# Optimization experiments

Measured on AMD Instinct MI355X. Metric: run time of the kernel, lower is better.

## Reference

```python
import jax, jax.numpy as jnp
import numpy as np

DMODEL = 1024
NHEAD = 16
DHEAD = DMODEL // NHEAD

def _layernorm(x, g, b, eps=1e-5):
    mu = jnp.mean(x, axis=-1, keepdims=True)
    var = jnp.var(x, axis=-1, keepdims=True)
    return (x - mu) * jax.lax.rsqrt(var + eps) * g + b

def setup_inputs() -> dict:
    key = jax.random.key(0)
    ks = jax.random.split(key, 12)
    b, lq, lv, d = 2, 2048, 2048, DMODEL
    s = 1.0 / np.sqrt(d)
    return {
        "q": jax.random.normal(ks[0], (b, lq, d), jnp.float32),
        "k": jax.random.normal(ks[1], (b, lv, d), jnp.float32),
        "v": jax.random.normal(ks[2], (b, lv, d), jnp.float32),
        "qln_g": jnp.ones((d,), jnp.float32),
        "qln_b": jnp.zeros((d,), jnp.float32),
        "kvln_g": jnp.ones((d,), jnp.float32),
        "kvln_b": jnp.zeros((d,), jnp.float32),
        "Wq": jax.random.normal(ks[3], (d, d), jnp.float32) * s,
        "Wk": jax.random.normal(ks[4], (d, d), jnp.float32) * s,
        "Wv": jax.random.normal(ks[5], (d, d), jnp.float32) * s,
        "Wg": jax.random.normal(ks[6], (d, d), jnp.float32) * s,
        "bg": jnp.zeros((d,), jnp.float32),
        "Wo": jax.random.normal(ks[7], (d, d), jnp.float32) * s,
    }

def reference(q, k, v, qln_g, qln_b, kvln_g, kvln_b, Wq, Wk, Wv, Wg, bg, Wo):
    b, lq, d = q.shape
    lv = v.shape[1]
    qn = _layernorm(q, qln_g, qln_b)           # [b, lq, d]
    q_ = qn @ Wq.T
    kk = _layernorm(k, kvln_g, kvln_b) @ Wk.T
    vv = _layernorm(v, kvln_g, kvln_b) @ Wv.T
    qh = q_.reshape(b, lq, NHEAD, DHEAD)       # bqhd
    kh = kk.reshape(b, lv, NHEAD, DHEAD)
    vh = vv.reshape(b, lv, NHEAD, DHEAD)
    scores = jnp.einsum('bqhd,bkhd->bhqk', qh, kh) / np.sqrt(DHEAD)
    attn = jax.nn.softmax(scores, axis=-1)
    y = jnp.einsum('bhqk,bkhd->bqhd', attn, vh).reshape(b, lq, d)
    g = jax.nn.sigmoid(qn @ Wg.T + bg)
    return (y * g) @ Wo.T
```

## Files before the change

kernel.cpp:

```cpp
#include <hip/hip_runtime.h>
#include <hip/hip_bf16.h>

#define DMODEL 1024
#define NHEAD  16
#define DHEAD  64
#define BATCH  2
#define LQ     2048
#define LV     2048
#define ROWS   (BATCH*LQ)
#define WELEMS (DMODEL*DMODEL)
#define BH     (BATCH*NHEAD)

typedef short bf16x8 __attribute__((ext_vector_type(8)));
typedef float f32x4  __attribute__((ext_vector_type(4)));

__device__ __forceinline__ float bf2f(unsigned short s) {
    union { unsigned u; float f; } v; v.u = ((unsigned)s) << 16;
    return v.f;
}
__device__ __forceinline__ unsigned pk_bf(float a, float b) {
    union { __hip_bfloat162 h; unsigned u; } c;
    c.h = __float22bfloat162_rn(make_float2(a, b));
    return c.u;
}

__device__ __forceinline__ void cp16_g2l(const void* g, void* l) {
    __builtin_amdgcn_global_load_lds(
        (const __attribute__((address_space(1))) void*)g,
        (__attribute__((address_space(3))) void*)l,
        16, 0, 0);
}

#define QSCALE (0.125f * 1.4426950408889634f)

__global__ __launch_bounds__(256) void prep_kernel(
    const float* q, const float* k, const float* v,
    const float* qg, const float* qb, const float* kvg, const float* kvb,
    const float* Wq, const float* Wk, const float* Wv, const float* Wg, const float* Wo,
    unsigned short* qn, unsigned short* kn, unsigned short* vn, unsigned short* wb)
{
    __shared__ float rs[4], rq[4];
    int z = blockIdx.y;
    if (z < 5) {
        if (blockIdx.x >= WELEMS / 1024) return;
        const float* srcs[5] = {Wq, Wk, Wv, Wg, Wo};
        const float* s = srcs[z];
        unsigned short* d = wb + (size_t)z * WELEMS;
        int i = (blockIdx.x * 256 + threadIdx.x) * 4;
        float4 x = *(const float4*)(s + i);
        uint2 o = make_uint2(pk_bf(x.x, x.y), pk_bf(x.z, x.w));
        *(uint2*)(d + i) = o;
        return;
    }
    int row = blockIdx.x;
    const float *x, *gp, *bp; unsigned short* o;
    if      (z == 5) { x = q; gp = qg;  bp = qb;  o = qn; }
    else if (z == 6) { x = k; gp = kvg; bp = kvb; o = kn; }
    else             { x = v; gp = kvg; bp = kvb; o = vn; }

    int col = threadIdx.x * 4;
    float4 xv = *(const float4*)(x + (size_t)row * DMODEL + col);
    float s  = xv.x + xv.y + xv.z + xv.w;
    float sq = xv.x*xv.x + xv.y*xv.y + xv.z*xv.z + xv.w*xv.w;
    #pragma unroll
    for (int off = 1; off < 64; off <<= 1) { s += __shfl_xor(s, off); sq += __shfl_xor(sq, off); }

    int wave = threadIdx.x >> 6, lane = threadIdx.x & 63;
    if (lane == 0) { rs[wave] = s; rq[wave] = sq; }
    __syncthreads();
    float ts = rs[0] + rs[1] + rs[2] + rs[3];
    float tq = rq[0] + rq[1] + rq[2] + rq[3];
    float mu  = ts * (1.0f / DMODEL);
    float var = tq * (1.0f / DMODEL) - mu * mu;
    float inv = rsqrtf(var + 1e-5f);

    float4 gv = *(const float4*)(gp + col);
    float4 bv = *(const float4*)(bp + col);
    float r0 = (xv.x - mu) * inv * gv.x + bv.x;
    float r1 = (xv.y - mu) * inv * gv.y + bv.y;
    float r2 = (xv.z - mu) * inv * gv.z + bv.z;
    float r3 = (xv.w - mu) * inv * gv.w + bv.w;
    *(uint2*)(o + (size_t)row * DMODEL + col) = make_uint2(pk_bf(r0, r1), pk_bf(r2, r3));
}

template<int MODE>
__device__ __forceinline__ void gemm256_core(
    const unsigned short* A, const unsigned short* Bw,
    unsigned short* Obf, const float* bias, float scale,
    unsigned short* Al, unsigned short* Bl, int bm, int bn)
{
    int tid  = threadIdx.x;
    int w = tid >> 6, l = tid & 63, quad = l >> 4, L = l & 15;
    int wm = w >> 2, wn = w & 3;

    int c16 = (l & 7) ^ (l >> 3);
    const unsigned short* gAs = A  + (size_t)(bm * 256 + w * 8 + (l >> 3)) * DMODEL + c16 * 8;
    const unsigned short* gBs = Bw + (size_t)(bn * 256 + w * 8 + (l >> 3)) * DMODEL + c16 * 8;
    int dstE = w * 512;

    #define STG_A2(t, ro) do { const unsigned short* s_ = gAs + (size_t)(ro) * DMODEL + (t) * 64; \
        unsigned short* d_ = Al + ((t) & 1) * 16384 + (ro) * 64 + dstE;                           \
        cp16_g2l(s_, d_); cp16_g2l(s_ + 64 * DMODEL, d_ + 4096); } while (0)
    #define STG_B2(t, ro) do { const unsigned short* s_ = gBs + (size_t)(ro) * DMODEL + (t) * 64; \
        unsigned short* d_ = Bl + ((t) & 1) * 16384 + (ro) * 64 + dstE;                           \
        cp16_g2l(s_, d_); cp16_g2l(s_ + 64 * DMODEL, d_ + 4096); } while (0)

    int sw = (L & 7) << 3;
    int o0 = (quad * 8) ^ sw;
    int o1 = (32 + quad * 8) ^ sw;

    f32x4 acc[8][4];
    #pragma unroll
    for (int i = 0; i < 8; ++i)
        #pragma unroll
        for (int j = 0; j < 4; ++j) acc[i][j] = (f32x4){0.f, 0.f, 0.f, 0.f};

    STG_A2(0, 0); STG_A2(0, 128); STG_B2(0, 0); STG_B2(0, 128);
    STG_A2(1, 0); STG_A2(1, 128);
    asm volatile("s_waitcnt vmcnt(4)" ::: "memory");
    __builtin_amdgcn_s_barrier();

    const int NT = DMODEL / 64;
    for (int t = 0; t < NT; ++t) {
        const unsigned short* Ab = Al + (t & 1) * 16384 + wm * 8192;
        const unsigned short* Bb = Bl + (t & 1) * 16384 + wn * 4096;
        bf16x8 b0[4], b1[4], a0[2], a1[2], r0v[6], r1v[6];

        #pragma unroll
        for (int j = 0; j < 4; ++j) {
            b0[j] = *(const bf16x8*)&Bb[(j * 16 + L) * 64 + o0];
            b1[j] = *(const bf16x8*)&Bb[(j * 16 + L) * 64 + o1];
        }
        #pragma unroll
        for (int i2 = 0; i2 < 2; ++i2) {
            a0[i2] = *(const bf16x8*)&Ab[(i2 * 16 + L) * 64 + o0];
            a1[i2] = *(const bf16x8*)&Ab[(i2 * 16 + L) * 64 + o1];
        }
        if (t + 1 < NT) STG_B2(t + 1, 0);
        __builtin_amdgcn_s_barrier();
        __builtin_amdgcn_s_setprio(1);
        #pragma unroll
        for (int i2 = 0; i2 < 2; ++i2)
            #pragma unroll
            for (int j = 0; j < 4; ++j) {
                if (MODE == 3) {
                    acc[i2][j] = __builtin_amdgcn_mfma_f32_16x16x32_bf16(a0[i2], b0[j], acc[i2][j], 0, 0, 0);
                    acc[i2][j] = __builtin_amdgcn_mfma_f32_16x16x32_bf16(a1[i2], b1[j], acc[i2][j], 0, 0, 0);
                } else {
                    acc[i2][j] = __builtin_amdgcn_mfma_f32_16x16x32_bf16(b0[j], a0[i2], acc[i2][j], 0, 0, 0);
                    acc[i2][j] = __builtin_amdgcn_mfma_f32_16x16x32_bf16(b1[j], a1[i2], acc[i2][j], 0, 0, 0);
                }
            }
        __builtin_amdgcn_s_setprio(0);
        __builtin_amdgcn_s_barrier();

        #pragma unroll
        for (int r = 0; r < 6; ++r) {
            r0v[r] = *(const bf16x8*)&Ab[((32 + r * 16) + L) * 64 + o0];
            r1v[r] = *(const bf16x8*)&Ab[((32 + r * 16) + L) * 64 + o1];
        }
        if (t + 1 < NT) STG_B2(t + 1, 128);
        __builtin_amdgcn_s_barrier();
        __builtin_amdgcn_s_setprio(1);
        #pragma unroll
        for (int i2 = 0; i2 < 2; ++i2)
            #pragma unroll
            for (int j = 0; j < 4; ++j) {
                if (MODE == 3) {
                    acc[2 + i2][j] = __builtin_amdgcn_mfma_f32_16x16x32_bf16(r0v[i2], b0[j], acc[2 + i2][j], 0, 0, 0);
                    acc[2 + i2][j] = __builtin_amdgcn_mfma_f32_16x16x32_bf16(r1v[i2], b1[j], acc[2 + i2][j], 0, 0, 0);
                } else {
                    acc[2 + i2][j] = __builtin_amdgcn_mfma_f32_16x16x32_bf16(b0[j], r0v[i2], acc[2 + i2][j], 0, 0, 0);
                    acc[2 + i2][j] = __builtin_amdgcn_mfma_f32_16x16x32_bf16(b1[j], r1v[i2], acc[2 + i2][j], 0, 0, 0);
                }
            }
        __builtin_amdgcn_s_setprio(0);
        asm volatile("s_waitcnt lgkmcnt(0)" ::: "memory");
        __builtin_amdgcn_sched_barrier(0);
        __builtin_amdgcn_s_barrier();

        if (t + 2 < NT) { STG_A2(t + 2, 0); STG_A2(t + 2, 128); }
        __builtin_amdgcn_s_barrier();
        __builtin_amdgcn_s_setprio(1);
        #pragma unroll
        for (int i2 = 0; i2 < 4; ++i2)
            #pragma unroll
            for (int j = 0; j < 4; ++j) {
                if (MODE == 3) {
                    acc[4 + i2][j] = __builtin_amdgcn_mfma_f32_16x16x32_bf16(r0v[2 + i2], b0[j], acc[4 + i2][j], 0, 0, 0);
                    acc[4 + i2][j] = __builtin_amdgcn_mfma_f32_16x16x32_bf16(r1v[2 + i2], b1[j], acc[4 + i2][j], 0, 0, 0);
                } else {
                    acc[4 + i2][j] = __builtin_amdgcn_mfma_f32_16x16x32_bf16(b0[j], r0v[2 + i2], acc[4 + i2][j], 0, 0, 0);
                    acc[4 + i2][j] = __builtin_amdgcn_mfma_f32_16x16x32_bf16(b1[j], r1v[2 + i2], acc[4 + i2][j], 0, 0, 0);
                }
            }
        __builtin_amdgcn_s_setprio(0);
        if (t + 2 < NT) asm volatile("s_waitcnt vmcnt(4)" ::: "memory");
        else            asm volatile("s_waitcnt vmcnt(0)" ::: "memory");
        __builtin_amdgcn_s_barrier();
    }
    #undef STG_A2
    #undef STG_B2

    #pragma unroll
    for (int i = 0; i < 8; ++i) {
        #pragma unroll
        for (int j = 0; j < 4; ++j) {
            f32x4 a = acc[i][j];
            if (MODE == 3) {
                int gcol  = bn * 256 + wn * 64 + j * 16 + L;
                int grow0 = bm * 256 + wm * 128 + i * 16 + quad * 4;
                int b = grow0 >> 11, key0 = grow0 & 2047;
                int h = gcol >> 6,   dd   = gcol & 63;
                uint2 o = make_uint2(pk_bf(a[0], a[1]), pk_bf(a[2], a[3]));
                *(uint2*)&Obf[(((size_t)(b * NHEAD + h) * DHEAD + dd) << 11) + key0] = o;
            } else {
                int grow  = bm * 256 + wm * 128 + i * 16 + L;
                int gcol0 = bn * 256 + wn * 64 + j * 16 + quad * 4;
                size_t idx = (size_t)grow * DMODEL + gcol0;
                if (MODE == 0) {
                    uint2 o = make_uint2(pk_bf(a[0] * scale, a[1] * scale),
                                         pk_bf(a[2] * scale, a[3] * scale));
                    *(uint2*)&Obf[idx] = o;
                } else {
                    float4 bv = *(const float4*)&bias[gcol0];
                    float s0 = 1.0f / (1.0f + __expf(-(a[0] + bv.x)));
                    float s1 = 1.0f / (1.0f + __expf(-(a[1] + bv.y)));
                    float s2 = 1.0f / (1.0f + __expf(-(a[2] + bv.z)));
                    float s3 = 1.0f / (1.0f + __expf(-(a[3] + bv.w)));
                    *(uint2*)&Obf[idx] = make_uint2(pk_bf(s0, s1), pk_bf(s2, s3));
                }
            }
        }
    }
}

__global__ __launch_bounds__(512, 2) void gemm256_kernel(
    const unsigned short* qn, const unsigned short* kn, const unsigned short* vn,
    const unsigned short* wb,
    unsigned short* qs, unsigned short* kkp, unsigned short* vt, unsigned short* gate,
    const float* bg)
{
    __shared__ __align__(16) unsigned short Al[2 * 256 * 64];
    __shared__ __align__(16) unsigned short Bl[2 * 256 * 64];
    int f = blockIdx.x, xcd = f & 7, s = f >> 3;
    int z  = xcd & 3;
    int bm = ((xcd >> 2) << 3) | (s >> 2);
    int bn = s & 3;
    switch (z) {
        case 0:  gemm256_core<0>(qn, wb + 0 * WELEMS, qs,   nullptr, QSCALE, Al, Bl, bm, bn); break;
        case 1:  gemm256_core<0>(kn, wb + 1 * WELEMS, kkp,  nullptr, 1.0f,   Al, Bl, bm, bn); break;
        case 2:  gemm256_core<3>(vn, wb + 2 * WELEMS, vt,   nullptr, 1.0f,   Al, Bl, bm, bn); break;
        default: gemm256_core<1>(qn, wb + 3 * WELEMS, gate, bg,      1.0f,   Al, Bl, bm, bn); break;
    }
}

template<int MODE>
__device__ __forceinline__ void gemm_bt_core(
    const unsigned short* A, const unsigned short* Bw,
    unsigned short* Obf, float* Of32, const float* bias, float scale,
    unsigned short* Al, unsigned short* Bl, int bm, int bn)
{
    int tid  = threadIdx.x;
    int wave = tid >> 6, lane = tid & 63, quad = lane >> 4, L = lane & 15;
    int wm = wave >> 1, wn = wave & 1;

    int srow = wave * 16 + (lane >> 2);
    int scol = (lane & 3) * 8;
    const unsigned short* gA = A  + (size_t)(bm * 128 + srow) * DMODEL + scol;
    const unsigned short* gB = Bw + (size_t)(bn * 128 + srow) * DMODEL + scol;
    int lofs0 = wave * 16 * 32;
    int lofs1 = (64 + wave * 16) * 32;

    f32x4 acc[4][4];
    #pragma unroll
    for (int i = 0; i < 4; ++i)
        #pragma unroll
        for (int j = 0; j < 4; ++j) acc[i][j] = (f32x4){0.f, 0.f, 0.f, 0.f};

    cp16_g2l(gA,               Al + lofs0);
    cp16_g2l(gA + 64 * DMODEL, Al + lofs1);
    cp16_g2l(gB,               Bl + lofs0);
    cp16_g2l(gB + 64 * DMODEL, Bl + lofs1);

    int buf = 0;
    for (int k0 = 0; k0 < DMODEL; k0 += 32, buf ^= 1) {
        __syncthreads();
        if (k0 + 32 < DMODEL) {
            int nb = (buf ^ 1) * (128 * 32);
            cp16_g2l(gA + k0 + 32,               Al + nb + lofs0);
            cp16_g2l(gA + 64 * DMODEL + k0 + 32, Al + nb + lofs1);
            cp16_g2l(gB + k0 + 32,               Bl + nb + lofs0);
            cp16_g2l(gB + 64 * DMODEL + k0 + 32, Bl + nb + lofs1);
        }
        const unsigned short* Ab = Al + buf * (128 * 32);
        const unsigned short* Bb = Bl + buf * (128 * 32);
        bf16x8 af[4], bfr[4];
        #pragma unroll
        for (int i = 0; i < 4; ++i)
            af[i] = *(const bf16x8*)&Ab[(wm * 64 + i * 16 + L) * 32 + quad * 8];
        #pragma unroll
        for (int j = 0; j < 4; ++j)
            bfr[j] = *(const bf16x8*)&Bb[(wn * 64 + j * 16 + L) * 32 + quad * 8];
        #pragma unroll
        for (int i = 0; i < 4; ++i)
            #pragma unroll
            for (int j = 0; j < 4; ++j) {
                if (MODE == 3)
                    acc[i][j] = __builtin_amdgcn_mfma_f32_16x16x32_bf16(af[i], bfr[j], acc[i][j], 0, 0, 0);
                else
                    acc[i][j] = __builtin_amdgcn_mfma_f32_16x16x32_bf16(bfr[j], af[i], acc[i][j], 0, 0, 0);
            }
    }

    #pragma unroll
    for (int i = 0; i < 4; ++i) {
        #pragma unroll
        for (int j = 0; j < 4; ++j) {
            f32x4 a = acc[i][j];
            int grow  = bm * 128 + wm * 64 + i * 16 + L;
            int gcol0 = bn * 128 + wn * 64 + j * 16 + quad * 4;
            size_t idx = (size_t)grow * DMODEL + gcol0;
            if (MODE == 2) {
                *(f32x4*)&Of32[idx] = a;
            } else if (MODE == 0) {
                uint2 o = make_uint2(pk_bf(a[0] * scale, a[1] * scale),
                                     pk_bf(a[2] * scale, a[3] * scale));
                *(uint2*)&Obf[idx] = o;
            }
        }
    }
}

__device__ __forceinline__ void xcd_map(int& bm, int& bn) {
    int f = blockIdx.y * 8 + blockIdx.x;
    int xcd = f & 7, s = f >> 3;
    bn = s & 7;
    bm = ((s >> 3) << 3) | xcd;
}

__global__ __launch_bounds__(256) void gemm_f32out_kernel(
    const unsigned short* A, const unsigned short* Bw, float* O)
{
    __shared__ __align__(16) unsigned short Al[2 * 128 * 32];
    __shared__ __align__(16) unsigned short Bl[2 * 128 * 32];
    int bm, bn; xcd_map(bm, bn);
    gemm_bt_core<2>(A, Bw, nullptr, O, nullptr, 1.0f, Al, Bl, bm, bn);
}

__global__ __launch_bounds__(256, 4) void attn_kernel(
    const unsigned short* qs, const unsigned short* kk, const unsigned short* vt,
    const unsigned short* gate, unsigned short* yg)
{
    __shared__ __align__(16) unsigned short Kl[2 * 64 * 64];
    __shared__ __align__(16) unsigned short Vl[3 * 64 * 64];

    int tid  = threadIdx.x;
    int wave = tid >> 6, lane = tid & 63, quad = lane >> 4, L = lane & 15;

    int f  = blockIdx.y * 32 + blockIdx.x;
    int bh = (f & 7) * 4 + ((f >> 3) & 3);
    int qt = f >> 5;
    int bb = bh >> 4, h = bh & 15;
    int q0 = qt * 64;

    const unsigned short* Qb =
        qs + ((size_t)(bb * LQ + q0 + wave * 16 + L)) * DMODEL + h * DHEAD;
    bf16x8 aq0 = *(const bf16x8*)(Qb + quad * 8);
    bf16x8 aq1 = *(const bf16x8*)(Qb + 32 + quad * 8);

    f32x4 acc[4];
    #pragma unroll
    for (int nt = 0; nt < 4; ++nt) acc[nt] = (f32x4){0.f, 0.f, 0.f, 0.f};
    f32x4 lacc = (f32x4){0.f, 0.f, 0.f, 0.f};
    bf16x8 ones;
    #pragma unroll
    for (int j = 0; j < 8; ++j) ones[j] = (short)0x3F80;

    int rloc = lane >> 3;
    int c16  = (lane & 7) ^ rloc;
    int key0 = (wave & 1) * 32 + (rloc >> 2) * 8 + (wave >> 1) * 4 + (rloc & 3);

    const unsigned short* gK = kk + (size_t)bb * LV * DMODEL + h * DHEAD
                                  + (size_t)key0 * DMODEL + c16 * 8;
    const unsigned short* gV = vt + ((size_t)((bb * NHEAD + h) * DHEAD
                                  + wave * 16 + rloc)) * LV + c16 * 8;
    char* KlB = (char*)Kl;
    char* VlB = (char*)Vl;
    int dst0 = wave * 2048;

    int sl0 = (quad ^ (L & 7)) * 8;

    cp16_g2l(gK,               KlB + dst0);
    cp16_g2l(gK + 16 * DMODEL, KlB + dst0 + 1024);
    cp16_g2l(gV,               VlB + dst0);
    cp16_g2l(gV + 8 * LV,      VlB + dst0 + 1024);
    __syncthreads();
    gK += 64 * DMODEL; gV += 64;
    cp16_g2l(gK,               KlB + 8192 + dst0);
    cp16_g2l(gK + 16 * DMODEL, KlB + 8192 + dst0 + 1024);
    cp16_g2l(gV,               VlB + 8192 + dst0);
    cp16_g2l(gV + 8 * LV,      VlB + 8192 + dst0 + 1024);

    bf16x8 pap0, pap1;

    {
        const unsigned short* Kb = Kl;
        f32x4 zz[4];
        __builtin_amdgcn_s_setprio(1);
        #pragma unroll
        for (int kt = 0; kt < 4; ++kt) {
            bf16x8 bk0 = *(const bf16x8*)&Kb[(kt * 16 + L) * 64 + sl0];
            bf16x8 bk1 = *(const bf16x8*)&Kb[(kt * 16 + L) * 64 + (sl0 ^ 32)];
            f32x4 z = (f32x4){0.f, 0.f, 0.f, 0.f};
            z = __builtin_amdgcn_mfma_f32_16x16x32_bf16(bk0, aq0, z, 0, 0, 0);
            z = __builtin_amdgcn_mfma_f32_16x16x32_bf16(bk1, aq1, z, 0, 0, 0);
            zz[kt] = z;
        }
        __builtin_amdgcn_s_setprio(0);
        union { unsigned u[4]; bf16x8 h; } pa0, pa1;
        pa0.u[0] = pk_bf(__builtin_amdgcn_exp2f(zz[0][0]), __builtin_amdgcn_exp2f(zz[0][1]));
        pa0.u[1] = pk_bf(__builtin_amdgcn_exp2f(zz[0][2]), __builtin_amdgcn_exp2f(zz[0][3]));
        pa0.u[2] = pk_bf(__builtin_amdgcn_exp2f(zz[2][0]), __builtin_amdgcn_exp2f(zz[2][1]));
        pa0.u[3] = pk_bf(__builtin_amdgcn_exp2f(zz[2][2]), __builtin_amdgcn_exp2f(zz[2][3]));
        pa1.u[0] = pk_bf(__builtin_amdgcn_exp2f(zz[1][0]), __builtin_amdgcn_exp2f(zz[1][1]));
        pa1.u[1] = pk_bf(__builtin_amdgcn_exp2f(zz[1][2]), __builtin_amdgcn_exp2f(zz[1][3]));
        pa1.u[2] = pk_bf(__builtin_amdgcn_exp2f(zz[3][0]), __builtin_amdgcn_exp2f(zz[3][1]));
        pa1.u[3] = pk_bf(__builtin_amdgcn_exp2f(zz[3][2]), __builtin_amdgcn_exp2f(zz[3][3]));
        pap0 = pa0.h; pap1 = pa1.h;
    }

    const int NT = LV / 64;
    int vs = 2;
    int vr = 0;
    for (int t = 1; t < NT; ++t) {
        __syncthreads();
        if (t + 1 < NT) {
            gK += 64 * DMODEL; gV += 64;
            int kb = ((t + 1) & 1) * 8192;
            cp16_g2l(gK,               KlB + kb + dst0);
            cp16_g2l(gK + 16 * DMODEL, KlB + kb + dst0 + 1024);
            int vb_ = vs * 8192;
            cp16_g2l(gV,               VlB + vb_ + dst0);
            cp16_g2l(gV + 8 * LV,      VlB + vb_ + dst0 + 1024);
            vs = (vs == 2) ? 0 : vs + 1;
        }
        const unsigned short* Vb = Vl + vr * 4096;
        vr = (vr == 2) ? 0 : vr + 1;
        const unsigned short* Kb = Kl + (t & 1) * 4096;

        bf16x8 vf0[4], vf1[4];
        #pragma unroll
        for (int nt = 0; nt < 4; ++nt) {
            vf0[nt] = *(const bf16x8*)&Vb[(nt * 16 + L) * 64 + sl0];
            vf1[nt] = *(const bf16x8*)&Vb[(nt * 16 + L) * 64 + (sl0 ^ 32)];
        }
        bf16x8 kf0[4], kf1[4];
        #pragma unroll
        for (int kt = 0; kt < 4; ++kt) {
            kf0[kt] = *(const bf16x8*)&Kb[(kt * 16 + L) * 64 + sl0];
            kf1[kt] = *(const bf16x8*)&Kb[(kt * 16 + L) * 64 + (sl0 ^ 32)];
        }

        __builtin_amdgcn_s_setprio(1);
        lacc = __builtin_amdgcn_mfma_f32_16x16x32_bf16(ones, pap0, lacc, 0, 0, 0);
        lacc = __builtin_amdgcn_mfma_f32_16x16x32_bf16(ones, pap1, lacc, 0, 0, 0);
        #pragma unroll
        for (int nt = 0; nt < 4; ++nt) {
            acc[nt] = __builtin_amdgcn_mfma_f32_16x16x32_bf16(vf0[nt], pap0, acc[nt], 0, 0, 0);
            acc[nt] = __builtin_amdgcn_mfma_f32_16x16x32_bf16(vf1[nt], pap1, acc[nt], 0, 0, 0);
        }
        f32x4 zz[4];
        #pragma unroll
        for (int kt = 0; kt < 4; ++kt) {
            f32x4 z = (f32x4){0.f, 0.f, 0.f, 0.f};
            z = __builtin_amdgcn_mfma_f32_16x16x32_bf16(kf0[kt], aq0, z, 0, 0, 0);
            z = __builtin_amdgcn_mfma_f32_16x16x32_bf16(kf1[kt], aq1, z, 0, 0, 0);
            zz[kt] = z;
        }
        __builtin_amdgcn_s_setprio(0);
        union { unsigned u[4]; bf16x8 h; } pa0, pa1;
        pa0.u[0] = pk_bf(__builtin_amdgcn_exp2f(zz[0][0]), __builtin_amdgcn_exp2f(zz[0][1]));
        pa0.u[1] = pk_bf(__builtin_amdgcn_exp2f(zz[0][2]), __builtin_amdgcn_exp2f(zz[0][3]));
        pa0.u[2] = pk_bf(__builtin_amdgcn_exp2f(zz[2][0]), __builtin_amdgcn_exp2f(zz[2][1]));
        pa0.u[3] = pk_bf(__builtin_amdgcn_exp2f(zz[2][2]), __builtin_amdgcn_exp2f(zz[2][3]));
        pa1.u[0] = pk_bf(__builtin_amdgcn_exp2f(zz[1][0]), __builtin_amdgcn_exp2f(zz[1][1]));
        pa1.u[1] = pk_bf(__builtin_amdgcn_exp2f(zz[1][2]), __builtin_amdgcn_exp2f(zz[1][3]));
        pa1.u[2] = pk_bf(__builtin_amdgcn_exp2f(zz[3][0]), __builtin_amdgcn_exp2f(zz[3][1]));
        pa1.u[3] = pk_bf(__builtin_amdgcn_exp2f(zz[3][2]), __builtin_amdgcn_exp2f(zz[3][3]));
        pap0 = pa0.h; pap1 = pa1.h;
    }

    {
        const unsigned short* Vb = Vl + 1 * 4096;
        bf16x8 vf0[4], vf1[4];
        #pragma unroll
        for (int nt = 0; nt < 4; ++nt) {
            vf0[nt] = *(const bf16x8*)&Vb[(nt * 16 + L) * 64 + sl0];
            vf1[nt] = *(const bf16x8*)&Vb[(nt * 16 + L) * 64 + (sl0 ^ 32)];
        }
        lacc = __builtin_amdgcn_mfma_f32_16x16x32_bf16(ones, pap0, lacc, 0, 0, 0);
        lacc = __builtin_amdgcn_mfma_f32_16x16x32_bf16(ones, pap1, lacc, 0, 0, 0);
        #pragma unroll
        for (int nt = 0; nt < 4; ++nt) {
            acc[nt] = __builtin_amdgcn_mfma_f32_16x16x32_bf16(vf0[nt], pap0, acc[nt], 0, 0, 0);
            acc[nt] = __builtin_amdgcn_mfma_f32_16x16x32_bf16(vf1[nt], pap1, acc[nt], 0, 0, 0);
        }
    }

    float inv_l = 1.0f / lacc[0];
    size_t rb = ((size_t)(bb * LQ + q0 + wave * 16 + L)) * DMODEL + h * DHEAD;
    #pragma unroll
    for (int nt = 0; nt < 4; ++nt) {
        size_t idx = rb + nt * 16 + quad * 4;
        ushort4 g = *(const ushort4*)&gate[idx];
        float y0 = acc[nt][0] * inv_l * bf2f(g.x);
        float y1 = acc[nt][1] * inv_l * bf2f(g.y);
        float y2 = acc[nt][2] * inv_l * bf2f(g.z);
        float y3 = acc[nt][3] * inv_l * bf2f(g.w);
        *(uint2*)&yg[idx] = make_uint2(pk_bf(y0, y1), pk_bf(y2, y3));
    }
}

extern "C" void kernel_launch(void* const* d_in, const int* in_sizes, int n_in,
                              void* d_out, int out_size, void* d_ws, size_t ws_size,
                              hipStream_t stream)
{
    const float* q      = (const float*)d_in[0];
    const float* k      = (const float*)d_in[1];
    const float* v      = (const float*)d_in[2];
    const float* qln_g  = (const float*)d_in[3];
    const float* qln_b  = (const float*)d_in[4];
    const float* kvln_g = (const float*)d_in[5];
    const float* kvln_b = (const float*)d_in[6];
    const float* Wq     = (const float*)d_in[7];
    const float* Wk     = (const float*)d_in[8];
    const float* Wv     = (const float*)d_in[9];
    const float* Wg     = (const float*)d_in[10];
    const float* bg     = (const float*)d_in[11];
    const float* Wo     = (const float*)d_in[12];
    float* out = (float*)d_out;

    const size_t T8 = (size_t)ROWS * DMODEL * 2;
    char* ws = (char*)d_ws;
    unsigned short* qn   = (unsigned short*)(ws + 0 * T8);
    unsigned short* kn   = (unsigned short*)(ws + 1 * T8);
    unsigned short* vn   = (unsigned short*)(ws + 2 * T8);
    unsigned short* qs   = (unsigned short*)(ws + 3 * T8);
    unsigned short* kkp  = (unsigned short*)(ws + 4 * T8);
    unsigned short* vt   = (unsigned short*)(ws + 5 * T8);
    unsigned short* gate = (unsigned short*)(ws + 6 * T8);
    unsigned short* yg   = (unsigned short*)(ws + 7 * T8);
    unsigned short* wb   = (unsigned short*)(ws + 8 * T8);

    prep_kernel<<<dim3(ROWS, 8), 256, 0, stream>>>(
        q, k, v, qln_g, qln_b, kvln_g, kvln_b, Wq, Wk, Wv, Wg, Wo, qn, kn, vn, wb);
    gemm256_kernel<<<dim3(256), 512, 0, stream>>>(
        qn, kn, vn, wb, qs, kkp, vt, gate, bg);
    attn_kernel<<<dim3(32, 32), 256, 0, stream>>>(qs, kkp, vt, gate, yg);
    gemm_f32out_kernel<<<dim3(DMODEL / 128, ROWS / 128), 256, 0, stream>>>(yg, wb + 4 * WELEMS, out);
}
```

Before: 227.9 us.

## Rework output GEMM with BK=64 swizzled pipeline and compact prep kernel grid

New measurement: 226.2 us. No clear change (-0.7%).

```diff
diff --git a/kernel.cpp b/kernel.cpp
--- a/kernel.cpp
+++ b/kernel.cpp
@@ -33,54 +33,65 @@
 
 #define QSCALE (0.125f * 1.4426950408889634f)
 
+#define PREP_WBLK (5 * 256)
+#define PREP_NBLK (PREP_WBLK + 3 * ROWS / 4)
+
 __global__ __launch_bounds__(256) void prep_kernel(
     const float* q, const float* k, const float* v,
     const float* qg, const float* qb, const float* kvg, const float* kvb,
     const float* Wq, const float* Wk, const float* Wv, const float* Wg, const float* Wo,
     unsigned short* qn, unsigned short* kn, unsigned short* vn, unsigned short* wb)
 {
-    __shared__ float rs[4], rq[4];
-    int z = blockIdx.y;
-    if (z < 5) {
-        if (blockIdx.x >= WELEMS / 1024) return;
+    int bx = blockIdx.x, tid = threadIdx.x;
+    if (bx < PREP_WBLK) {
+        int z = bx >> 8;
         const float* srcs[5] = {Wq, Wk, Wv, Wg, Wo};
-        const float* s = srcs[z];
-        unsigned short* d = wb + (size_t)z * WELEMS;
-        int i = (blockIdx.x * 256 + threadIdx.x) * 4;
-        float4 x = *(const float4*)(s + i);
-        uint2 o = make_uint2(pk_bf(x.x, x.y), pk_bf(x.z, x.w));
-        *(uint2*)(d + i) = o;
+        size_t base = (size_t)(bx & 255) * 4096;
+        const float* s = srcs[z] + base;
+        unsigned short* d = wb + (size_t)z * WELEMS + base;
+        #pragma unroll
+        for (int u = 0; u < 4; ++u) {
+            int i = u * 1024 + tid * 4;
+            float4 x = *(const float4*)(s + i);
+            *(uint2*)(d + i) = make_uint2(pk_bf(x.x, x.y), pk_bf(x.z, x.w));
+        }
         return;
     }
-    int row = blockIdx.x;
+    int wave = tid >> 6, lane = tid & 63;
+    int gr = (bx - PREP_WBLK) * 4 + wave;
+    int tz = gr >> 12, row = gr & 4095;
     const float *x, *gp, *bp; unsigned short* o;
-    if      (z == 5) { x = q; gp = qg;  bp = qb;  o = qn; }
-    else if (z == 6) { x = k; gp = kvg; bp = kvb; o = kn; }
-    else             { x = v; gp = kvg; bp = kvb; o = vn; }
-
-    int col = threadIdx.x * 4;
-    float4 xv = *(const float4*)(x + (size_t)row * DMODEL + col);
-    float s  = xv.x + xv.y + xv.z + xv.w;
-    float sq = xv.x*xv.x + xv.y*xv.y + xv.z*xv.z + xv.w*xv.w;
+    if      (tz == 0) { x = q; gp = qg;  bp = qb;  o = qn; }
+    else if (tz == 1) { x = k; gp = kvg; bp = kvb; o = kn; }
+    else              { x = v; gp = kvg; bp = kvb; o = vn; }
+    const float* xr = x + (size_t)row * DMODEL;
+
+    float4 xv[4];
+    float s = 0.f, sq = 0.f;
+    #pragma unroll
+    for (int u = 0; u < 4; ++u) {
+        xv[u] = *(const float4*)(xr + u * 256 + lane * 4);
+        s  += xv[u].x + xv[u].y + xv[u].z + xv[u].w;
+        sq += xv[u].x*xv[u].x + xv[u].y*xv[u].y + xv[u].z*xv[u].z + xv[u].w*xv[u].w;
+    }
     #pragma unroll
     for (int off = 1; off < 64; off <<= 1) { s += __shfl_xor(s, off); sq += __shfl_xor(sq, off); }
-
-    int wave = threadIdx.x >> 6, lane = threadIdx.x & 63;
-    if (lane == 0) { rs[wave] = s; rq[wave] = sq; }
-    __syncthreads();
-    float ts = rs[0] + rs[1] + rs[2] + rs[3];
-    float tq = rq[0] + rq[1] + rq[2] + rq[3];
-    float mu  = ts * (1.0f / DMODEL);
-    float var = tq * (1.0f / DMODEL) - mu * mu;
+    float mu  = s * (1.0f / DMODEL);
+    float var = sq * (1.0f / DMODEL) - mu * mu;
     float inv = rsqrtf(var + 1e-5f);
 
-    float4 gv = *(const float4*)(gp + col);
-    float4 bv = *(const float4*)(bp + col);
-    float r0 = (xv.x - mu) * inv * gv.x + bv.x;
-    float r1 = (xv.y - mu) * inv * gv.y + bv.y;
-    float r2 = (xv.z - mu) * inv * gv.z + bv.z;
-    float r3 = (xv.w - mu) * inv * gv.w + bv.w;
-    *(uint2*)(o + (size_t)row * DMODEL + col) = make_uint2(pk_bf(r0, r1), pk_bf(r2, r3));
+    unsigned short* orow = o + (size_t)row * DMODEL;
+    #pragma unroll
+    for (int u = 0; u < 4; ++u) {
+        int col = u * 256 + lane * 4;
+        float4 gv = *(const float4*)(gp + col);
+        float4 bv = *(const float4*)(bp + col);
+        float r0 = (xv[u].x - mu) * inv * gv.x + bv.x;
+        float r1 = (xv[u].y - mu) * inv * gv.y + bv.y;
+        float r2 = (xv[u].z - mu) * inv * gv.z + bv.z;
+        float r3 = (xv[u].w - mu) * inv * gv.w + bv.w;
+        *(uint2*)(orow + col) = make_uint2(pk_bf(r0, r1), pk_bf(r2, r3));
+    }
 }
 
 template<int MODE>
@@ -255,83 +266,6 @@
     }
 }
 
-template<int MODE>
-__device__ __forceinline__ void gemm_bt_core(
-    const unsigned short* A, const unsigned short* Bw,
-    unsigned short* Obf, float* Of32, const float* bias, float scale,
-    unsigned short* Al, unsigned short* Bl, int bm, int bn)
-{
-    int tid  = threadIdx.x;
-    int wave = tid >> 6, lane = tid & 63, quad = lane >> 4, L = lane & 15;
-    int wm = wave >> 1, wn = wave & 1;
-
-    int srow = wave * 16 + (lane >> 2);
-    int scol = (lane & 3) * 8;
-    const unsigned short* gA = A  + (size_t)(bm * 128 + srow) * DMODEL + scol;
-    const unsigned short* gB = Bw + (size_t)(bn * 128 + srow) * DMODEL + scol;
-    int lofs0 = wave * 16 * 32;
-    int lofs1 = (64 + wave * 16) * 32;
-
-    f32x4 acc[4][4];
-    #pragma unroll
-    for (int i = 0; i < 4; ++i)
-        #pragma unroll
-        for (int j = 0; j < 4; ++j) acc[i][j] = (f32x4){0.f, 0.f, 0.f, 0.f};
-
-    cp16_g2l(gA,               Al + lofs0);
-    cp16_g2l(gA + 64 * DMODEL, Al + lofs1);
-    cp16_g2l(gB,               Bl + lofs0);
-    cp16_g2l(gB + 64 * DMODEL, Bl + lofs1);
-
-    int buf = 0;
-    for (int k0 = 0; k0 < DMODEL; k0 += 32, buf ^= 1) {
-        __syncthreads();
-        if (k0 + 32 < DMODEL) {
-            int nb = (buf ^ 1) * (128 * 32);
-            cp16_g2l(gA + k0 + 32,               Al + nb + lofs0);
-            cp16_g2l(gA + 64 * DMODEL + k0 + 32, Al + nb + lofs1);
-            cp16_g2l(gB + k0 + 32,               Bl + nb + lofs0);
-            cp16_g2l(gB + 64 * DMODEL + k0 + 32, Bl + nb + lofs1);
-        }
-        const unsigned short* Ab = Al + buf * (128 * 32);
-        const unsigned short* Bb = Bl + buf * (128 * 32);
-        bf16x8 af[4], bfr[4];
-        #pragma unroll
-        for (int i = 0; i < 4; ++i)
-            af[i] = *(const bf16x8*)&Ab[(wm * 64 + i * 16 + L) * 32 + quad * 8];
-        #pragma unroll
-        for (int j = 0; j < 4; ++j)
-            bfr[j] = *(const bf16x8*)&Bb[(wn * 64 + j * 16 + L) * 32 + quad * 8];
-        #pragma unroll
-        for (int i = 0; i < 4; ++i)
-            #pragma unroll
-            for (int j = 0; j < 4; ++j) {
-                if (MODE == 3)
-                    acc[i][j] = __builtin_amdgcn_mfma_f32_16x16x32_bf16(af[i], bfr[j], acc[i][j], 0, 0, 0);
-                else
-                    acc[i][j] = __builtin_amdgcn_mfma_f32_16x16x32_bf16(bfr[j], af[i], acc[i][j], 0, 0, 0);
-            }
-    }
-
-    #pragma unroll
-    for (int i = 0; i < 4; ++i) {
-        #pragma unroll
-        for (int j = 0; j < 4; ++j) {
-            f32x4 a = acc[i][j];
-            int grow  = bm * 128 + wm * 64 + i * 16 + L;
-            int gcol0 = bn * 128 + wn * 64 + j * 16 + quad * 4;
-            size_t idx = (size_t)grow * DMODEL + gcol0;
-            if (MODE == 2) {
-                *(f32x4*)&Of32[idx] = a;
-            } else if (MODE == 0) {
-                uint2 o = make_uint2(pk_bf(a[0] * scale, a[1] * scale),
-                                     pk_bf(a[2] * scale, a[3] * scale));
-                *(uint2*)&Obf[idx] = o;
-            }
-        }
-    }
-}
-
 __device__ __forceinline__ void xcd_map(int& bm, int& bn) {
     int f = blockIdx.y * 8 + blockIdx.x;
     int xcd = f & 7, s = f >> 3;
@@ -339,13 +273,85 @@
     bm = ((s >> 3) << 3) | xcd;
 }
 
-__global__ __launch_bounds__(256) void gemm_f32out_kernel(
+__global__ __launch_bounds__(256, 2) void gemm_f32out_kernel(
     const unsigned short* A, const unsigned short* Bw, float* O)
 {
-    __shared__ __align__(16) unsigned short Al[2 * 128 * 32];
-    __shared__ __align__(16) unsigned short Bl[2 * 128 * 32];
+    __shared__ __align__(16) unsigned short Al[2 * 128 * 64];
+    __shared__ __align__(16) unsigned short Bl[2 * 128 * 64];
     int bm, bn; xcd_map(bm, bn);
-    gemm_bt_core<2>(A, Bw, nullptr, O, nullptr, 1.0f, Al, Bl, bm, bn);
+    int tid = threadIdx.x;
+    int w = tid >> 6, l = tid & 63, quad = l >> 4, L = l & 15;
+    int wm = w >> 1, wn = w & 1;
+
+    int c16 = (l & 7) ^ (l >> 3);
+    const unsigned short* gAs = A  + (size_t)(bm * 128 + w * 8 + (l >> 3)) * DMODEL + c16 * 8;
+    const unsigned short* gBs = Bw + (size_t)(bn * 128 + w * 8 + (l >> 3)) * DMODEL + c16 * 8;
+    int dstE = w * 512;
+
+    #define STG4(t, gp, lp) do { const unsigned short* s_ = (gp) + (t) * 64;  \
+        unsigned short* d_ = (lp) + ((t) & 1) * 8192 + dstE;                  \
+        cp16_g2l(s_,               d_);                                       \
+        cp16_g2l(s_ + 32 * DMODEL, d_ + 2048);                                \
+        cp16_g2l(s_ + 64 * DMODEL, d_ + 4096);                                \
+        cp16_g2l(s_ + 96 * DMODEL, d_ + 6144); } while (0)
+
+    int sw = (L & 7) << 3;
+    int o0 = (quad * 8) ^ sw;
+    int o1 = (32 + quad * 8) ^ sw;
+
+    f32x4 acc[4][4];
+    #pragma unroll
+    for (int i = 0; i < 4; ++i)
+        #pragma unroll
+        for (int j = 0; j < 4; ++j) acc[i][j] = (f32x4){0.f, 0.f, 0.f, 0.f};
+
+    STG4(0, gAs, Al); STG4(0, gBs, Bl);
+
+    const int NT = DMODEL / 64;
+    for (int t = 0; t < NT; ++t) {
+        if (t + 1 < NT) {
+            STG4(t + 1, gAs, Al); STG4(t + 1, gBs, Bl);
+            asm volatile("s_waitcnt vmcnt(8)" ::: "memory");
+        } else {
+            asm volatile("s_waitcnt vmcnt(0)" ::: "memory");
+        }
+        __builtin_amdgcn_s_barrier();
+
+        const unsigned short* Ab = Al + (t & 1) * 8192 + (wm * 64) * 64;
+        const unsigned short* Bb = Bl + (t & 1) * 8192 + (wn * 64) * 64;
+        bf16x8 a0[4], a1[4], b0[4], b1[4];
+        #pragma unroll
+        for (int j = 0; j < 4; ++j) {
+            b0[j] = *(const bf16x8*)&Bb[(j * 16 + L) * 64 + o0];
+            b1[j] = *(const bf16x8*)&Bb[(j * 16 + L) * 64 + o1];
+        }
+        #pragma unroll
+        for (int i = 0; i < 4; ++i) {
+            a0[i] = *(const bf16x8*)&Ab[(i * 16 + L) * 64 + o0];
+            a1[i] = *(const bf16x8*)&Ab[(i * 16 + L) * 64 + o1];
+        }
+        __builtin_amdgcn_s_setprio(1);
+        #pragma unroll
+        for (int i = 0; i < 4; ++i)
+            #pragma unroll
+            for (int j = 0; j < 4; ++j) {
+                acc[i][j] = __builtin_amdgcn_mfma_f32_16x16x32_bf16(b0[j], a0[i], acc[i][j], 0, 0, 0);
+                acc[i][j] = __builtin_amdgcn_mfma_f32_16x16x32_bf16(b1[j], a1[i], acc[i][j], 0, 0, 0);
+            }
+        __builtin_amdgcn_s_setprio(0);
+        __builtin_amdgcn_s_barrier();
+    }
+    #undef STG4
+
+    #pragma unroll
+    for (int i = 0; i < 4; ++i) {
+        #pragma unroll
+        for (int j = 0; j < 4; ++j) {
+            int grow  = bm * 128 + wm * 64 + i * 16 + L;
+            int gcol0 = bn * 128 + wn * 64 + j * 16 + quad * 4;
+            *(f32x4*)&O[(size_t)grow * DMODEL + gcol0] = acc[i][j];
+        }
+    }
 }
 
 __global__ __launch_bounds__(256, 4) void attn_kernel(
@@ -553,7 +559,7 @@
     unsigned short* yg   = (unsigned short*)(ws + 7 * T8);
     unsigned short* wb   = (unsigned short*)(ws + 8 * T8);
 
-    prep_kernel<<<dim3(ROWS, 8), 256, 0, stream>>>(
+    prep_kernel<<<dim3(PREP_NBLK), 256, 0, stream>>>(
         q, k, v, qln_g, qln_b, kvln_g, kvln_b, Wq, Wk, Wv, Wg, Wo, qn, kn, vn, wb);
     gemm256_kernel<<<dim3(256), 512, 0, stream>>>(
         qn, kn, vn, wb, qs, kkp, vt, gate, bg);
```
